# Kernel optimization log

Measured on AMD Instinct MI355X. Metric: run time of the kernel, lower is better.

Reference implementation:

```python
import jax, jax.numpy as jnp
import numpy as np

N = 100000      # nodes
E = 1600000     # directed edges
F_IN = 128      # input features
H = 64          # hidden_channels
C = 32          # num_classes


def setup_inputs() -> dict:
    key = jax.random.key(0)
    ks = jax.random.split(key, 8)
    x = jax.random.normal(ks[0], (N, F_IN), jnp.float32)
    edge_index = jax.random.randint(ks[1], (2, E), 0, N, jnp.int32)
    W1 = jax.random.normal(ks[2], (F_IN, H), jnp.float32) * (1.0 / np.sqrt(F_IN))
    b1 = jnp.zeros((H,), jnp.float32)
    W2 = jax.random.normal(ks[3], (H, H), jnp.float32) * (1.0 / np.sqrt(H))
    b2 = jnp.zeros((H,), jnp.float32)
    Wout = jax.random.normal(ks[4], (H, C), jnp.float32) * (1.0 / np.sqrt(H))
    bout = jnp.zeros((C,), jnp.float32)
    return {"x": x, "edge_index": edge_index, "W1": W1, "b1": b1,
            "W2": W2, "b2": b2, "Wout": Wout, "bout": bout}


def gcn_conv(x, W, b, src, dst, n):
    """PyG GCNConv: out = D^-1/2 (A + I) D^-1/2 (X W) + b,
    with degree computed on A + I."""
    h = x @ W  # [N, out]
    ones = jnp.ones(dst.shape[0], h.dtype)
    deg = jax.ops.segment_sum(ones, dst, num_segments=n) + 1.0  # self-loop
    dinv = jax.lax.rsqrt(deg)                                   # [N]
    coef = dinv[src] * dinv[dst]                                # [E]
    agg = jax.ops.segment_sum(h[src] * coef[:, None], dst, num_segments=n)
    agg = agg + h * (dinv * dinv)[:, None]                      # self-loop message
    return agg + b


def reference(x, edge_index, W1, b1, W2, b2, Wout, bout):
    src, dst = edge_index[0], edge_index[1]
    n = x.shape[0]
    h = jax.nn.relu(gcn_conv(x, W1, b1, src, dst, n))
    # dropout(p=0.5) is a no-op in eval mode
    h = jax.nn.relu(gcn_conv(h, W2, b2, src, dst, n))
    return jax.nn.softmax(h @ Wout + bout, axis=1)
```

## Files before the change

### kernel.cpp

```cpp
#include <hip/hip_runtime.h>
#include <stdint.h>


typedef unsigned short u16;
typedef unsigned int u32;
typedef __attribute__((ext_vector_type(8))) short bf16x8;
typedef __attribute__((ext_vector_type(4))) float f32x4;
typedef __attribute__((ext_vector_type(2))) float f32x2;

#define GN 100000
#define GE 1600000
#define NBKT 196
#define BCAP 10240
#define EBLK 782

__device__ __forceinline__ float bf2f(u32 lo16) {
  union { u32 i; float f; } v; v.i = lo16 << 16; return v.f;
}
__device__ __forceinline__ u16 f2bf(float f) {
  union { float f; u32 i; } v; v.f = f;
  u32 x = v.i;
  u32 r = x + 0x7fffu + ((x >> 16) & 1u);
  return (u16)(r >> 16);
}
__device__ __forceinline__ u32 pack2(float a, float b) {
  return (u32)f2bf(a) | ((u32)f2bf(b) << 16);
}
__device__ __forceinline__ f32x2 unpk(u32 u) {
  union { u32 i; float f; } lo, hi;
  lo.i = u << 16; hi.i = u & 0xffff0000u;
  return (f32x2){lo.f, hi.f};
}

__global__ __launch_bounds__(256) void k_detect(const u16* __restrict__ xs,
                                                int* __restrict__ flag,
                                                int* __restrict__ ccount) {
  __shared__ int cnt;
  if (threadIdx.x == 0) cnt = 0;
  if (threadIdx.x < NBKT) ccount[threadIdx.x] = 0;
  __syncthreads();
  int w = 0;
#pragma unroll
  for (int i = 0; i < 16; i++) {
    int s = threadIdx.x * 16 + i;
    u32 u = xs[(size_t)s * 1562];
    u32 ex = (u >> 7) & 0xffu;
    if (ex == 0xffu || ex < 0x40u) w++;
  }
  atomicAdd(&cnt, w);
  __syncthreads();
  if (threadIdx.x == 0) flag[0] = (cnt >= 64) ? 0 : 1;
}

__global__ __launch_bounds__(256) void k_partA(const int* __restrict__ src,
                                               const int* __restrict__ dst,
                                               int* __restrict__ ccount, int E,
                                               const void* p2, const void* p3,
                                               const void* p4, const void* p5,
                                               const void* p6, const void* p7,
                                               const int* __restrict__ flag,
                                               float* __restrict__ Wf,
                                               u16* __restrict__ Wb1,
                                               u16* __restrict__ Wb2,
                                               u16* __restrict__ Wbo,
                                               u32* __restrict__ pairs) {
  int tid = threadIdx.x;
  if (blockIdx.x >= EBLK) {
    int i = (blockIdx.x - EBLK) * 256 + tid;
    bool isbf = flag[0] != 0;
    if (i < 14496) {
      const void* sp; int off;
      if (i < 8192)       { sp = p2; off = i; }
      else if (i < 8256)  { sp = p3; off = i - 8192; }
      else if (i < 12352) { sp = p4; off = i - 8256; }
      else if (i < 12416) { sp = p5; off = i - 12352; }
      else if (i < 14464) { sp = p6; off = i - 12416; }
      else                { sp = p7; off = i - 14464; }
      Wf[i] = isbf ? bf2f((u32)((const u16*)sp)[off]) : ((const float*)sp)[off];
    } else if (i < 14496 + 12288) {
      int idx = i - 14496;
      const void* W; u16* dstp;
      if (idx < 8192) { W = p2; dstp = Wb1; }
      else            { W = p4; dstp = Wb2; idx -= 8192; }
      int j  = idx & 7;
      int l  = (idx >> 3) & 63;
      int c  = (idx >> 9) & 3;
      int kc = idx >> 11;
      int k = kc * 32 + (l >> 4) * 8 + j;
      int n = c * 16 + (l & 15);
      dstp[idx] = isbf ? ((const u16*)W)[k * 64 + n]
                       : f2bf(((const float*)W)[k * 64 + n]);
    } else if (i < 14496 + 12288 + 2048) {
      int idx = i - 14496 - 12288;
      int j  = idx & 7;
      int l  = (idx >> 3) & 63;
      int c  = (idx >> 9) & 1;
      int kc = idx >> 10;
      int k = kc * 32 + (l >> 4) * 8 + j;
      int n = c * 16 + (l & 15);
      Wbo[idx] = isbf ? ((const u16*)p6)[k * 32 + n]
                      : f2bf(((const float*)p6)[k * 32 + n]);
    }
    return;
  }
  __shared__ int hist[256];
  __shared__ int boff[256];
  __shared__ int fill[256];
  __shared__ int gbase[256];
  __shared__ int sc[256];
  __shared__ u32 buf[2048];
  __shared__ int adr[2048];
  __shared__ int stotal;
  hist[tid] = 0;
  __syncthreads();
  int e0 = (blockIdx.x * 256 + tid) * 8;
  int s_[8], d_[8];
  int cnt = 0;
  if (e0 + 8 <= E) {
    const int4* sp = (const int4*)(src + e0);
    const int4* dp = (const int4*)(dst + e0);
#pragma unroll
    for (int q = 0; q < 2; q++) {
      int4 sv = sp[q], dv = dp[q];
      s_[4 * q + 0] = sv.x; s_[4 * q + 1] = sv.y;
      s_[4 * q + 2] = sv.z; s_[4 * q + 3] = sv.w;
      d_[4 * q + 0] = dv.x; d_[4 * q + 1] = dv.y;
      d_[4 * q + 2] = dv.z; d_[4 * q + 3] = dv.w;
    }
    cnt = 8;
  } else {
    for (int q = 0; q < 8 && e0 + q < E; q++) {
      s_[q] = src[e0 + q]; d_[q] = dst[e0 + q]; cnt++;
    }
  }
  for (int q = 0; q < cnt; q++) atomicAdd(&hist[d_[q] >> 9], 1);
  __syncthreads();
  int v = hist[tid];
  sc[tid] = v;
  __syncthreads();
#pragma unroll
  for (int off = 1; off < 256; off <<= 1) {
    int a = (tid >= off) ? sc[tid - off] : 0;
    __syncthreads();
    sc[tid] += a;
    __syncthreads();
  }
  int excl = sc[tid] - v;
  boff[tid] = excl;
  fill[tid] = excl;
  if (tid == 255) stotal = sc[255];
  if (tid < NBKT && v > 0) gbase[tid] = tid * BCAP + atomicAdd(&ccount[tid], v);
  __syncthreads();
  for (int q = 0; q < cnt; q++) {
    int bkt = d_[q] >> 9;
    int p = atomicAdd(&fill[bkt], 1);
    buf[p] = ((u32)s_[q] << 9) | ((u32)d_[q] & 511u);
    adr[p] = gbase[bkt] + (p - boff[bkt]);
  }
  __syncthreads();
  int total = stotal;
  for (int j = tid; j < total; j += 256) pairs[adr[j]] = buf[j];
}

__global__ __launch_bounds__(256) void k_partB(const u32* __restrict__ pairs,
                                               const int* __restrict__ ccount,
                                               int* __restrict__ rpx,
                                               float* __restrict__ dinv,
                                               int* __restrict__ ssort, int N) {
  __shared__ int cnt[512];
  __shared__ int sc[256];
  int b = blockIdx.x;
  int tid = threadIdx.x;
  int nb0 = b << 9;
  int beg = b * BCAP, end = beg + ccount[b];
  cnt[tid] = 0; cnt[tid + 256] = 0;
  __syncthreads();
  for (int i = beg + tid; i < end; i += 256) {
    u32 p = pairs[i];
    atomicAdd(&cnt[p & 511u], 1);
  }
  __syncthreads();
  int c0 = cnt[2 * tid], c1 = cnt[2 * tid + 1];
  int s = c0 + c1;
  sc[tid] = s;
  __syncthreads();
#pragma unroll
  for (int off = 1; off < 256; off <<= 1) {
    int a = (tid >= off) ? sc[tid - off] : 0;
    __syncthreads();
    sc[tid] += a;
    __syncthreads();
  }
  int excl = sc[tid] - s;
  cnt[2 * tid] = excl;
  cnt[2 * tid + 1] = excl + c0;
  int idx = b * 513 + 2 * tid;
  rpx[idx]     = beg + excl;
  rpx[idx + 1] = beg + excl + c0;
  if (tid == 255) rpx[b * 513 + 512] = end;
  int n0 = nb0 + 2 * tid, n1 = n0 + 1;
  if (n0 < N) dinv[n0] = rsqrtf((float)c0 + 1.0f);
  if (n1 < N) dinv[n1] = rsqrtf((float)c1 + 1.0f);
  __syncthreads();
  for (int i = beg + tid; i < end; i += 256) {
    u32 p = pairs[i];
    int pos = beg + atomicAdd(&cnt[p & 511u], 1);
    ssort[pos] = (int)(p >> 9);
  }
}

template <int K, int XMODE>
__global__ __launch_bounds__(256) void k_mgemm(const void* __restrict__ X,
                                               const u16* __restrict__ Wb,
                                               const float* __restrict__ dinv,
                                               const int* __restrict__ flag,
                                               u16* __restrict__ out, int M) {
  constexpr int NKC = K / 32;
  constexpr int P = K + 8;
  __shared__ u16 Bs[NKC * 4 * 64 * 8];
  __shared__ u16 As[128 * P];
  int tid = threadIdx.x;
  bool isbf = (XMODE == 1) ? true : (flag[0] != 0);
#pragma unroll
  for (int i = 0; i < NKC; i++)
    ((uint4*)Bs)[i * 256 + tid] = ((const uint4*)Wb)[i * 256 + tid];

  int rowbase = blockIdx.x * 128;
  int rowsValid = M - rowbase; if (rowsValid > 128) rowsValid = 128;
  if (isbf) {
    constexpr int F8 = K / 8;
    constexpr int NL = K / 16;
    const uint4* Xg = (const uint4*)X;
    uint4 v[NL];
#pragma unroll
    for (int i = 0; i < NL; i++) {
      int q = i * 256 + tid;
      int row = q / F8, c8 = q % F8;
      v[i] = (row < rowsValid) ? Xg[(size_t)(rowbase + row) * F8 + c8]
                               : make_uint4(0, 0, 0, 0);
    }
#pragma unroll
    for (int i = 0; i < NL; i++) {
      int q = i * 256 + tid;
      int row = q / F8, c8 = q % F8;
      *(uint4*)&As[row * P + c8 * 8] = v[i];
    }
  } else {
    constexpr int F4 = K / 4;
    constexpr int NL = K / 8;
    const float4* Xg = (const float4*)X;
    float4 v[NL];
#pragma unroll
    for (int i = 0; i < NL; i++) {
      int q = i * 256 + tid;
      int row = q / F4, c4 = q % F4;
      v[i] = (row < rowsValid) ? Xg[(size_t)(rowbase + row) * F4 + c4]
                               : make_float4(0.f, 0.f, 0.f, 0.f);
    }
#pragma unroll
    for (int i = 0; i < NL; i++) {
      int q = i * 256 + tid;
      int row = q / F4, c4 = q % F4;
      u32* d = (u32*)&As[row * P + c4 * 4];
      d[0] = pack2(v[i].x, v[i].y);
      d[1] = pack2(v[i].z, v[i].w);
    }
  }
  __syncthreads();

  int lane = tid & 63, wave = tid >> 6;
  int m0 = lane & 15;
  int koff = (lane >> 4) * 8;
  f32x4 acc[2][4];
#pragma unroll
  for (int t = 0; t < 2; t++)
#pragma unroll
    for (int c = 0; c < 4; c++) acc[t][c] = (f32x4){0.f, 0.f, 0.f, 0.f};

#pragma unroll
  for (int kc = 0; kc < NKC; kc++) {
    union { uint4 v; bf16x8 s; } a[2];
#pragma unroll
    for (int t = 0; t < 2; t++) {
      int rl = wave * 32 + t * 16 + m0;
      a[t].v = *(const uint4*)&As[rl * P + kc * 32 + koff];
    }
#pragma unroll
    for (int c = 0; c < 4; c++) {
      bf16x8 b = *(const bf16x8*)&Bs[((kc * 4 + c) * 64 + lane) * 8];
      acc[0][c] = __builtin_amdgcn_mfma_f32_16x16x32_bf16(a[0].s, b, acc[0][c], 0, 0, 0);
      acc[1][c] = __builtin_amdgcn_mfma_f32_16x16x32_bf16(a[1].s, b, acc[1][c], 0, 0, 0);
    }
  }
  __syncthreads();
  int cl = lane & 15, rq = (lane >> 4) * 4;
#pragma unroll
  for (int t = 0; t < 2; t++)
#pragma unroll
    for (int reg = 0; reg < 4; reg++) {
      int rl = wave * 32 + t * 16 + rq + reg;
      int r = rowbase + rl;
      float s = (r < M) ? dinv[r] : 0.f;
#pragma unroll
      for (int c = 0; c < 4; c++)
        As[rl * P + c * 16 + cl] = f2bf(acc[t][c][reg] * s);
    }
  __syncthreads();
  uint4* outg = (uint4*)out;
#pragma unroll
  for (int i = 0; i < 4; i++) {
    int q = i * 256 + tid;
    int row = q >> 3, c8 = q & 7;
    int r = rowbase + row;
    if (r < M) outg[(size_t)r * 8 + c8] = *(uint4*)&As[row * P + c8 * 8];
  }
}

template <int MODE>
__global__ __launch_bounds__(256) void k_pullg(const u16* __restrict__ g,
                                               const int* __restrict__ rpx,
                                               const int* __restrict__ ss,
                                               const float* __restrict__ dinv,
                                               const float* __restrict__ bias,
                                               const u16* __restrict__ Wfrag,
                                               const float* __restrict__ bof,
                                               const int* __restrict__ flag,
                                               void* __restrict__ outv) {
  constexpr int P = 72;
  __shared__ u16 Hs[32 * P];
  __shared__ u16 Cs[(MODE == 0) ? 32 * P : 1];
  int tid = threadIdx.x;
  int lane = tid & 63, wave = tid >> 6;

  constexpr int NCF = (MODE == 0) ? 4 : 2;
  int c0 = (MODE == 0) ? ((wave >> 1) << 1) : 0;
  bf16x8 bfr[2][2];
#pragma unroll
  for (int kc = 0; kc < 2; kc++)
#pragma unroll
    for (int cc = 0; cc < 2; cc++)
      bfr[kc][cc] = *(const bf16x8*)&Wfrag[((kc * NCF + c0 + cc) * 64 + lane) * 8];

  int oct = tid >> 3;
  int node = blockIdx.x * 32 + oct;
  int fq = tid & 7;
  const uint4* gp4 = (const uint4*)g;
  int rix = node + (node >> 9);
  int beg = rpx[rix], end = rpx[rix + 1];

  uint4 sv = gp4[(size_t)node * 8 + fq];
  f32x2 acc2[4];
  acc2[0] = unpk(sv.x); acc2[1] = unpk(sv.y);
  acc2[2] = unpk(sv.z); acc2[3] = unpk(sv.w);

#define ACC8(v)                                             \
  do {                                                      \
    acc2[0] += unpk((v).x); acc2[1] += unpk((v).y);         \
    acc2[2] += unpk((v).z); acc2[3] += unpk((v).w);         \
  } while (0)

  int e = beg;
  for (; e + 8 <= end; e += 8) {
    int i0 = ss[e],     i1 = ss[e + 1], i2 = ss[e + 2], i3 = ss[e + 3];
    int i4 = ss[e + 4], i5 = ss[e + 5], i6 = ss[e + 6], i7 = ss[e + 7];
    uint4 v0 = gp4[(size_t)i0 * 8 + fq];
    uint4 v1 = gp4[(size_t)i1 * 8 + fq];
    uint4 v2 = gp4[(size_t)i2 * 8 + fq];
    uint4 v3 = gp4[(size_t)i3 * 8 + fq];
    uint4 v4 = gp4[(size_t)i4 * 8 + fq];
    uint4 v5 = gp4[(size_t)i5 * 8 + fq];
    uint4 v6 = gp4[(size_t)i6 * 8 + fq];
    uint4 v7 = gp4[(size_t)i7 * 8 + fq];
    ACC8(v0); ACC8(v1); ACC8(v2); ACC8(v3);
    ACC8(v4); ACC8(v5); ACC8(v6); ACC8(v7);
  }
  if (e + 4 <= end) {
    int i0 = ss[e], i1 = ss[e + 1], i2 = ss[e + 2], i3 = ss[e + 3];
    uint4 v0 = gp4[(size_t)i0 * 8 + fq];
    uint4 v1 = gp4[(size_t)i1 * 8 + fq];
    uint4 v2 = gp4[(size_t)i2 * 8 + fq];
    uint4 v3 = gp4[(size_t)i3 * 8 + fq];
    ACC8(v0); ACC8(v1); ACC8(v2); ACC8(v3);
    e += 4;
  }
  for (; e < end; e++) {
    int i0 = ss[e];
    uint4 v0 = gp4[(size_t)i0 * 8 + fq];
    ACC8(v0);
  }
#undef ACC8

  float dv = dinv[node];
  float4 b0 = ((const float4*)bias)[fq * 2];
  float4 b1 = ((const float4*)bias)[fq * 2 + 1];
  float r0 = fmaxf(dv * acc2[0].x + b0.x, 0.f);
  float r1 = fmaxf(dv * acc2[0].y + b0.y, 0.f);
  float r2 = fmaxf(dv * acc2[1].x + b0.z, 0.f);
  float r3 = fmaxf(dv * acc2[1].y + b0.w, 0.f);
  float r4 = fmaxf(dv * acc2[2].x + b1.x, 0.f);
  float r5 = fmaxf(dv * acc2[2].y + b1.y, 0.f);
  float r6 = fmaxf(dv * acc2[3].x + b1.z, 0.f);
  float r7 = fmaxf(dv * acc2[3].y + b1.w, 0.f);
  *(uint4*)&Hs[oct * P + fq * 8] =
      make_uint4(pack2(r0, r1), pack2(r2, r3), pack2(r4, r5), pack2(r6, r7));
  __syncthreads();

  int m0 = lane & 15;
  int koff = (lane >> 4) * 8;
  int rt = wave & 1;
  f32x4 cacc[2];
  cacc[0] = (f32x4){0.f, 0.f, 0.f, 0.f};
  cacc[1] = (f32x4){0.f, 0.f, 0.f, 0.f};
  if (MODE == 0 || wave < 2) {
#pragma unroll
    for (int kc = 0; kc < 2; kc++) {
      union { uint4 v; bf16x8 s; } a;
      a.v = *(const uint4*)&Hs[(rt * 16 + m0) * P + kc * 32 + koff];
      cacc[0] = __builtin_amdgcn_mfma_f32_16x16x32_bf16(a.s, bfr[kc][0], cacc[0], 0, 0, 0);
      cacc[1] = __builtin_amdgcn_mfma_f32_16x16x32_bf16(a.s, bfr[kc][1], cacc[1], 0, 0, 0);
    }
  }
  int cl = lane & 15, rq = (lane >> 4) * 4;
  if (MODE == 0) {
#pragma unroll
    for (int reg = 0; reg < 4; reg++) {
      int rl = rt * 16 + rq + reg;
      float s = dinv[blockIdx.x * 32 + rl];
      Cs[rl * P + (c0 + 0) * 16 + cl] = f2bf(cacc[0][reg] * s);
      Cs[rl * P + (c0 + 1) * 16 + cl] = f2bf(cacc[1][reg] * s);
    }
    __syncthreads();
    uint4* og = (uint4*)outv;
    int row = tid >> 3, c8 = tid & 7;
    og[(size_t)(blockIdx.x * 32 + row) * 8 + c8] = *(uint4*)&Cs[row * P + c8 * 8];
  } else if (wave < 2) {
    bool isbf = flag[0] != 0;
    float bb0 = bof[cl], bb1 = bof[16 + cl];
#pragma unroll
    for (int reg = 0; reg < 4; reg++) {
      int r = blockIdx.x * 32 + rt * 16 + rq + reg;
      float v0 = cacc[0][reg] + bb0;
      float v1 = cacc[1][reg] + bb1;
      float mx = fmaxf(v0, v1);
      mx = fmaxf(mx, __shfl_xor(mx, 1));
      mx = fmaxf(mx, __shfl_xor(mx, 2));
      mx = fmaxf(mx, __shfl_xor(mx, 4));
      mx = fmaxf(mx, __shfl_xor(mx, 8));
      float e0 = __expf(v0 - mx), e1 = __expf(v1 - mx);
      float s = e0 + e1;
      s += __shfl_xor(s, 1);
      s += __shfl_xor(s, 2);
      s += __shfl_xor(s, 4);
      s += __shfl_xor(s, 8);
      float inv = 1.f / s;
      if (isbf) {
        u16* go = (u16*)outv;
        go[(size_t)r * 32 + cl]      = f2bf(e0 * inv);
        go[(size_t)r * 32 + 16 + cl] = f2bf(e1 * inv);
      } else {
        float* go = (float*)outv;
        go[(size_t)r * 32 + cl]      = e0 * inv;
        go[(size_t)r * 32 + 16 + cl] = e1 * inv;
      }
    }
  }
}

extern "C" void kernel_launch(void* const* d_in, const int* in_sizes, int n_in,
                              void* d_out, int out_size, void* d_ws, size_t ws_size,
                              hipStream_t stream) {
  (void)in_sizes; (void)n_in; (void)out_size; (void)ws_size;
  const void* x  = d_in[0];
  const int* ei  = (const int*)d_in[1];
  const int E = GE;
  const int* srcI = ei;
  const int* dstI = ei + E;

  char* ws = (char*)d_ws;
  int*   flag   = (int*)(ws + 0);
  int*   ccount = (int*)(ws + 256);
  int*   rpx    = (int*)(ws + 4096);
  float* dinv   = (float*)(ws + 406528);
  float* Wf     = (float*)(ws + 806656);
  u16*   Wb1    = (u16*)(ws + 864768);
  u16*   Wb2    = (u16*)(ws + 881280);
  u16*   Wbo    = (u16*)(ws + 889600);
  int*   ssort  = (int*)(ws + 893952);
  u32*   pairs  = (u32*)(ws + 8922112);
  u16*   gA     = (u16*)(ws + 8922112);
  u16*   gB     = (u16*)(ws + 21722368);

  float* b1f = Wf + 8192;
  float* b2f = Wf + 12352;
  float* bof = Wf + 14464;

  k_detect<<<1, 256, 0, stream>>>((const u16*)x, flag, ccount);
  k_partA<<<EBLK + 113, 256, 0, stream>>>(srcI, dstI, ccount, E,
                                          d_in[2], d_in[3], d_in[4], d_in[5],
                                          d_in[6], d_in[7], flag,
                                          Wf, Wb1, Wb2, Wbo, pairs);
  k_partB<<<NBKT, 256, 0, stream>>>(pairs, ccount, rpx, dinv, ssort, GN);

  k_mgemm<128, 0><<<782, 256, 0, stream>>>(x, Wb1, dinv, flag, gA, GN);
  k_pullg<0><<<3125, 256, 0, stream>>>(gA, rpx, ssort, dinv, b1f, Wb2, bof, flag, gB);
  k_pullg<1><<<3125, 256, 0, stream>>>(gB, rpx, ssort, dinv, b2f, Wbo, bof, flag, d_out);
}
```

Measured before the change: 236.2 us.

## Split each node's edge gather across two thread groups in pull kernels

The pull-aggregation kernels now handle 16 nodes per block instead of 32. Each node's edge range is split between two 8-thread groups, and the partial sums are combined with a cross-lane shuffle. This doubles the grid and the parallelism available for the latency-bound gather, aiming to hide memory latency and to even out degree imbalance. In exchange, fewer loads are in flight per thread (the unroll drops from 8 to 4), there are extra shuffles, and the MFMA stage is restructured so each wave computes one 16-column slice, which adds per-block overhead.

```diff
diff --git a/kernel.cpp b/kernel.cpp
--- a/kernel.cpp
+++ b/kernel.cpp
@@ -327,31 +327,25 @@
                                                const int* __restrict__ flag,
                                                void* __restrict__ outv) {
   constexpr int P = 72;
-  __shared__ u16 Hs[32 * P];
-  __shared__ u16 Cs[(MODE == 0) ? 32 * P : 1];
+  __shared__ u16 Hs[16 * P];
+  __shared__ u16 Cs[(MODE == 0) ? 16 * P : 1];
   int tid = threadIdx.x;
   int lane = tid & 63, wave = tid >> 6;
 
-  constexpr int NCF = (MODE == 0) ? 4 : 2;
-  int c0 = (MODE == 0) ? ((wave >> 1) << 1) : 0;
-  bf16x8 bfr[2][2];
-#pragma unroll
-  for (int kc = 0; kc < 2; kc++)
-#pragma unroll
-    for (int cc = 0; cc < 2; cc++)
-      bfr[kc][cc] = *(const bf16x8*)&Wfrag[((kc * NCF + c0 + cc) * 64 + lane) * 8];
-
-  int oct = tid >> 3;
-  int node = blockIdx.x * 32 + oct;
+  int nloc = tid >> 4;
+  int node = blockIdx.x * 16 + nloc;
+  int sub = (tid >> 3) & 1;
   int fq = tid & 7;
   const uint4* gp4 = (const uint4*)g;
   int rix = node + (node >> 9);
   int beg = rpx[rix], end = rpx[rix + 1];
-
-  uint4 sv = gp4[(size_t)node * 8 + fq];
+  int half = (end - beg + 1) >> 1;
+  int lo = beg + sub * half;
+  int hi = sub ? end : beg + half;
+
   f32x2 acc2[4];
-  acc2[0] = unpk(sv.x); acc2[1] = unpk(sv.y);
-  acc2[2] = unpk(sv.z); acc2[3] = unpk(sv.w);
+#pragma unroll
+  for (int j = 0; j < 4; j++) acc2[j] = (f32x2){0.f, 0.f};
 
 #define ACC8(v)                                             \
   do {                                                      \
@@ -359,86 +353,96 @@
     acc2[2] += unpk((v).z); acc2[3] += unpk((v).w);         \
   } while (0)
 
-  int e = beg;
-  for (; e + 8 <= end; e += 8) {
-    int i0 = ss[e],     i1 = ss[e + 1], i2 = ss[e + 2], i3 = ss[e + 3];
-    int i4 = ss[e + 4], i5 = ss[e + 5], i6 = ss[e + 6], i7 = ss[e + 7];
-    uint4 v0 = gp4[(size_t)i0 * 8 + fq];
-    uint4 v1 = gp4[(size_t)i1 * 8 + fq];
-    uint4 v2 = gp4[(size_t)i2 * 8 + fq];
-    uint4 v3 = gp4[(size_t)i3 * 8 + fq];
-    uint4 v4 = gp4[(size_t)i4 * 8 + fq];
-    uint4 v5 = gp4[(size_t)i5 * 8 + fq];
-    uint4 v6 = gp4[(size_t)i6 * 8 + fq];
-    uint4 v7 = gp4[(size_t)i7 * 8 + fq];
-    ACC8(v0); ACC8(v1); ACC8(v2); ACC8(v3);
-    ACC8(v4); ACC8(v5); ACC8(v6); ACC8(v7);
-  }
-  if (e + 4 <= end) {
+  int e = lo;
+  for (; e + 4 <= hi; e += 4) {
     int i0 = ss[e], i1 = ss[e + 1], i2 = ss[e + 2], i3 = ss[e + 3];
     uint4 v0 = gp4[(size_t)i0 * 8 + fq];
     uint4 v1 = gp4[(size_t)i1 * 8 + fq];
     uint4 v2 = gp4[(size_t)i2 * 8 + fq];
     uint4 v3 = gp4[(size_t)i3 * 8 + fq];
     ACC8(v0); ACC8(v1); ACC8(v2); ACC8(v3);
-    e += 4;
-  }
-  for (; e < end; e++) {
+  }
+  for (; e < hi; e++) {
     int i0 = ss[e];
     uint4 v0 = gp4[(size_t)i0 * 8 + fq];
     ACC8(v0);
   }
+  if (!sub) {
+    uint4 sv = gp4[(size_t)node * 8 + fq];
+    ACC8(sv);
+  }
 #undef ACC8
 
-  float dv = dinv[node];
-  float4 b0 = ((const float4*)bias)[fq * 2];
-  float4 b1 = ((const float4*)bias)[fq * 2 + 1];
-  float r0 = fmaxf(dv * acc2[0].x + b0.x, 0.f);
-  float r1 = fmaxf(dv * acc2[0].y + b0.y, 0.f);
-  float r2 = fmaxf(dv * acc2[1].x + b0.z, 0.f);
-  float r3 = fmaxf(dv * acc2[1].y + b0.w, 0.f);
-  float r4 = fmaxf(dv * acc2[2].x + b1.x, 0.f);
-  float r5 = fmaxf(dv * acc2[2].y + b1.y, 0.f);
-  float r6 = fmaxf(dv * acc2[3].x + b1.z, 0.f);
-  float r7 = fmaxf(dv * acc2[3].y + b1.w, 0.f);
-  *(uint4*)&Hs[oct * P + fq * 8] =
-      make_uint4(pack2(r0, r1), pack2(r2, r3), pack2(r4, r5), pack2(r6, r7));
+#pragma unroll
+  for (int j = 0; j < 4; j++) {
+    acc2[j].x += __shfl_xor(acc2[j].x, 8);
+    acc2[j].y += __shfl_xor(acc2[j].y, 8);
+  }
+
+  if (!(tid & 8)) {
+    float dv = dinv[node];
+    float4 b0 = ((const float4*)bias)[fq * 2];
+    float4 b1 = ((const float4*)bias)[fq * 2 + 1];
+    float r0 = fmaxf(dv * acc2[0].x + b0.x, 0.f);
+    float r1 = fmaxf(dv * acc2[0].y + b0.y, 0.f);
+    float r2 = fmaxf(dv * acc2[1].x + b0.z, 0.f);
+    float r3 = fmaxf(dv * acc2[1].y + b0.w, 0.f);
+    float r4 = fmaxf(dv * acc2[2].x + b1.x, 0.f);
+    float r5 = fmaxf(dv * acc2[2].y + b1.y, 0.f);
+    float r6 = fmaxf(dv * acc2[3].x + b1.z, 0.f);
+    float r7 = fmaxf(dv * acc2[3].y + b1.w, 0.f);
+    *(uint4*)&Hs[nloc * P + fq * 8] =
+        make_uint4(pack2(r0, r1), pack2(r2, r3), pack2(r4, r5), pack2(r6, r7));
+  }
   __syncthreads();
 
   int m0 = lane & 15;
   int koff = (lane >> 4) * 8;
-  int rt = wave & 1;
-  f32x4 cacc[2];
-  cacc[0] = (f32x4){0.f, 0.f, 0.f, 0.f};
-  cacc[1] = (f32x4){0.f, 0.f, 0.f, 0.f};
-  if (MODE == 0 || wave < 2) {
+  int cl = lane & 15, rq = (lane >> 4) * 4;
+  if (MODE == 0) {
+    int c0 = wave;
+    bf16x8 bf0 = *(const bf16x8*)&Wfrag[((0 * 4 + c0) * 64 + lane) * 8];
+    bf16x8 bf1 = *(const bf16x8*)&Wfrag[((1 * 4 + c0) * 64 + lane) * 8];
+    union { uint4 v; bf16x8 s; } a0, a1;
+    a0.v = *(const uint4*)&Hs[m0 * P + 0 + koff];
+    a1.v = *(const uint4*)&Hs[m0 * P + 32 + koff];
+    f32x4 cacc = (f32x4){0.f, 0.f, 0.f, 0.f};
+    cacc = __builtin_amdgcn_mfma_f32_16x16x32_bf16(a0.s, bf0, cacc, 0, 0, 0);
+    cacc = __builtin_amdgcn_mfma_f32_16x16x32_bf16(a1.s, bf1, cacc, 0, 0, 0);
+#pragma unroll
+    for (int reg = 0; reg < 4; reg++) {
+      int row = rq + reg;
+      float s = dinv[blockIdx.x * 16 + row];
+      Cs[row * P + c0 * 16 + cl] = f2bf(cacc[reg] * s);
+    }
+    __syncthreads();
+    if (tid < 128) {
+      int row = tid >> 3, c8 = tid & 7;
+      ((uint4*)outv)[(size_t)(blockIdx.x * 16 + row) * 8 + c8] =
+          *(uint4*)&Cs[row * P + c8 * 8];
+    }
+  } else if (wave == 0) {
+    bf16x8 bfr[2][2];
+#pragma unroll
+    for (int kc = 0; kc < 2; kc++)
+#pragma unroll
+      for (int cc = 0; cc < 2; cc++)
+        bfr[kc][cc] = *(const bf16x8*)&Wfrag[((kc * 2 + cc) * 64 + lane) * 8];
+    f32x4 cacc[2];
+    cacc[0] = (f32x4){0.f, 0.f, 0.f, 0.f};
+    cacc[1] = (f32x4){0.f, 0.f, 0.f, 0.f};
 #pragma unroll
     for (int kc = 0; kc < 2; kc++) {
       union { uint4 v; bf16x8 s; } a;
-      a.v = *(const uint4*)&Hs[(rt * 16 + m0) * P + kc * 32 + koff];
+      a.v = *(const uint4*)&Hs[m0 * P + kc * 32 + koff];
       cacc[0] = __builtin_amdgcn_mfma_f32_16x16x32_bf16(a.s, bfr[kc][0], cacc[0], 0, 0, 0);
       cacc[1] = __builtin_amdgcn_mfma_f32_16x16x32_bf16(a.s, bfr[kc][1], cacc[1], 0, 0, 0);
     }
-  }
-  int cl = lane & 15, rq = (lane >> 4) * 4;
-  if (MODE == 0) {
-#pragma unroll
-    for (int reg = 0; reg < 4; reg++) {
-      int rl = rt * 16 + rq + reg;
-      float s = dinv[blockIdx.x * 32 + rl];
-      Cs[rl * P + (c0 + 0) * 16 + cl] = f2bf(cacc[0][reg] * s);
-      Cs[rl * P + (c0 + 1) * 16 + cl] = f2bf(cacc[1][reg] * s);
-    }
-    __syncthreads();
-    uint4* og = (uint4*)outv;
-    int row = tid >> 3, c8 = tid & 7;
-    og[(size_t)(blockIdx.x * 32 + row) * 8 + c8] = *(uint4*)&Cs[row * P + c8 * 8];
-  } else if (wave < 2) {
     bool isbf = flag[0] != 0;
     float bb0 = bof[cl], bb1 = bof[16 + cl];
 #pragma unroll
     for (int reg = 0; reg < 4; reg++) {
-      int r = blockIdx.x * 32 + rt * 16 + rq + reg;
+      int r = blockIdx.x * 16 + rq + reg;
       float v0 = cacc[0][reg] + bb0;
       float v1 = cacc[1][reg] + bb1;
       float mx = fmaxf(v0, v1);
@@ -502,6 +506,6 @@
   k_partB<<<NBKT, 256, 0, stream>>>(pairs, ccount, rpx, dinv, ssort, GN);
 
   k_mgemm<128, 0><<<782, 256, 0, stream>>>(x, Wb1, dinv, flag, gA, GN);
-  k_pullg<0><<<3125, 256, 0, stream>>>(gA, rpx, ssort, dinv, b1f, Wb2, bof, flag, gB);
-  k_pullg<1><<<3125, 256, 0, stream>>>(gB, rpx, ssort, dinv, b2f, Wbo, bof, flag, d_out);
-}
+  k_pullg<0><<<6250, 256, 0, stream>>>(gA, rpx, ssort, dinv, b1f, Wb2, bof, flag, gB);
+  k_pullg<1><<<6250, 256, 0, stream>>>(gB, rpx, ssort, dinv, b2f, Wbo, bof, flag, d_out);
+}
```

After: 232.3 us. Within noise of the previous version (-1.6%).
